# Kernel tuning notes

Hardware: AMD Instinct MI355X
Metric: run time of the kernel (lower is better)

## Reference

```python
import jax, jax.numpy as jnp
import numpy as np


def setup_inputs() -> dict:
    key = jax.random.key(0)
    n, d = 256, 64
    ks = jax.random.split(key, 8)
    x = jax.random.normal(ks[0], (n, d), jnp.float32)
    v = jax.random.normal(ks[1], (n, d), jnp.float32)
    # torch nn.Linear convention: weight shape (out_features, in_features)
    W1 = jax.random.normal(ks[2], (d, d), jnp.float32) * (1.0 / np.sqrt(d))
    b1 = jax.random.normal(ks[3], (d,), jnp.float32) * 0.1
    # W2 scaled small + b2 ~ scaled identity so g = M + M^T is well-conditioned (invertible)
    W2 = jax.random.normal(ks[4], (d * d, d), jnp.float32) * 0.02
    b2 = (3.0 * jnp.eye(d, dtype=jnp.float32)).reshape(d * d) \
         + jax.random.normal(ks[5], (d * d,), jnp.float32) * 0.01
    W3 = jax.random.normal(ks[6], (d, 2 * d), jnp.float32) * (1.0 / np.sqrt(2 * d))
    return {"t": 0, "x": x, "v": v, "W1": W1, "b1": b1, "W2": W2, "b2": b2, "W3": W3}


def reference(t, x, v, W1, b1, W2, b2, W3):
    # Connection_gnew.forward. t is unused (ODE-time placeholder), matching the original.
    n, d = x.shape
    # g network: linear1 -> tanh -> linear2 -> symmetrize
    h = jnp.tanh(x @ W1.T + b1)                      # (n, d)
    M = (h @ W2.T + b2).reshape(n, d, d)             # (n, d, d)
    g = M + jnp.transpose(M, (0, 2, 1))              # symmetric metric (n, d, d)
    g_inv = jnp.linalg.inv(g)
    # Analytic batch jacobian of g_flat wrt x (replaces autograd.functional.jacobian):
    # d M_flat[a]/d x[l] = sum_m W2[a,m] * (1 - h[m]^2) * W1[m,l]; then symmetrize (i<->j).
    s = 1.0 - h * h                                   # tanh' (n, d)
    J = jnp.einsum('am,nm,ml->nal', W2, s, W1).reshape(n, d, d, d)
    J = J + jnp.transpose(J, (0, 2, 1, 3))            # J[n,i,j,l] = d g_{ij} / d x_l
    # einsum('nkl,nijl,njil,nlij->nkij', g_inv, J, J, -J):
    # elementwise triple product over matching indices, then contract l with g_inv.
    T = J * jnp.transpose(J, (0, 2, 1, 3)) * (-jnp.transpose(J, (0, 2, 3, 1)))  # T[n,i,j,l]
    connection = 0.5 * jnp.einsum('nkl,nijl->nkij', g_inv, T)
    # dv[n,k] = -sum_{ij} v_i v_j connection[n,k,i,j]
    dv = -jnp.einsum('ni,nj,nkij->nk', v, v, connection)
    out = jnp.concatenate([v, dv], axis=-1) @ W3.T    # linear3, no bias
    return out
```

## Files before the change

kernel.cpp:

```cpp
#include <hip/hip_runtime.h>
#include <math.h>
#include <stdint.h>


typedef short short8 __attribute__((ext_vector_type(8)));
typedef float f32x4 __attribute__((ext_vector_type(4)));
typedef float f32x2 __attribute__((ext_vector_type(2)));

__device__ __forceinline__ unsigned short f2bf(float f) {
  unsigned int u = __builtin_bit_cast(unsigned int, f);
  u += 0x7fffu + ((u >> 16) & 1u);
  return (unsigned short)(u >> 16);
}

__device__ __forceinline__ short8 as_short8(uint4 u) {
  union { uint4 a; short8 b; } cv; cv.a = u; return cv.b;
}

__device__ __forceinline__ void stage_slab(const unsigned short* gslab,
                                           unsigned short* lbase, int lane) {
  const int srcoff = ((lane >> 3) << 6) + (((lane & 7) ^ (lane >> 3)) << 3);
  const unsigned short* gsrc = gslab + srcoff;
  #pragma unroll
  for (int k = 0; k < 8; ++k) {
    __builtin_amdgcn_global_load_lds(
        (const __attribute__((address_space(1))) unsigned int*)(gsrc + (k << 9)),
        (__attribute__((address_space(3))) unsigned int*)(lbase + (k << 9)),
        16, 0, 0);
  }
}

__global__ __launch_bounds__(256) void prep_kernel(
    const float* __restrict__ W2, const float* __restrict__ W1,
    const float* __restrict__ b2, unsigned short* __restrict__ W2sB,
    float* __restrict__ W1T, float* __restrict__ b2s) {
  const int b = blockIdx.x;
  if (b < 128) {
    int g = b * 256 + threadIdx.x;
    int i = g >> 9, j = (g >> 3) & 63, m8 = (g & 7) << 3;
    const float* pa = &W2[((((i << 6) + j) << 6) + m8)];
    const float* pb = &W2[((((j << 6) + i) << 6) + m8)];
    float4 a0 = *(const float4*)pa, a1 = *(const float4*)(pa + 4);
    float4 b0 = *(const float4*)pb, b1 = *(const float4*)(pb + 4);
    short8 r;
    r[0] = (short)f2bf(a0.x + b0.x); r[1] = (short)f2bf(a0.y + b0.y);
    r[2] = (short)f2bf(a0.z + b0.z); r[3] = (short)f2bf(a0.w + b0.w);
    r[4] = (short)f2bf(a1.x + b1.x); r[5] = (short)f2bf(a1.y + b1.y);
    r[6] = (short)f2bf(a1.z + b1.z); r[7] = (short)f2bf(a1.w + b1.w);
    *(short8*)&W2sB[(size_t)g << 3] = r;
  } else if (b == 128) {
    for (int e = threadIdx.x; e < 4096; e += 256) {
      int l = e >> 6, m = e & 63;
      W1T[e] = W1[(m << 6) + l];
    }
  } else {
    for (int e = threadIdx.x; e < 4096; e += 256) {
      int r = e >> 6, c = e & 63;
      b2s[e] = b2[(r << 6) + c] + b2[(c << 6) + r];
    }
  }
}

__global__ __launch_bounds__(512) void conn_kernel(
    const float* __restrict__ x, const float* __restrict__ v,
    const float* __restrict__ W1, const float* __restrict__ b1,
    const float* __restrict__ W3, const unsigned short* __restrict__ W2sB,
    const float* __restrict__ W1T, const float* __restrict__ b2s,
    float* __restrict__ out) {
  __shared__ __align__(16) unsigned short sAF[8][2][4096];
  __shared__ __align__(16) unsigned short sKT[80 * 80];
  __shared__ __align__(16) float sg[64 * 68];
  __shared__ __align__(16) float sh[64], sv[64], sx[64];

  float* const spq = (float*)sKT;
  float* const sq  = (float*)sKT + 512;
  float* const szz = (float*)sKT + 576;

  const int n = blockIdx.x, t = threadIdx.x;
  const int wv = t >> 6, lane = t & 63, ln15 = lane & 15, quad = lane >> 4;
  const int o8 = t >> 3, s8 = t & 7;

  if (t < 64) sx[t] = x[(n << 6) + t];
  else if (t < 128) sv[t - 64] = v[(n << 6) + (t - 64)];
  for (int e = t; e < 1280; e += 512) sKT[5120 + e] = 0;
  __syncthreads();

  {
    const float* w1r = &W1[(o8 << 6) + (s8 << 3)];
    float4 wa = *(const float4*)w1r, wb = *(const float4*)(w1r + 4);
    float4 xa = *(const float4*)&sx[s8 << 3], xb = *(const float4*)&sx[(s8 << 3) + 4];
    float acc = wa.x * xa.x + wa.y * xa.y + wa.z * xa.z + wa.w * xa.w
              + wb.x * xb.x + wb.y * xb.y + wb.z * xb.z + wb.w * xb.w;
    acc += __shfl_xor(acc, 1);
    acc += __shfl_xor(acc, 2);
    acc += __shfl_xor(acc, 4);
    if (s8 == 0) sh[o8] = tanhf(acc + b1[o8]);
  }
  __syncthreads();

  for (int e = t; e < 4096; e += 512) {
    int m = e & 63, l = e >> 6;
    float hm = sh[m];
    sKT[l * 80 + m] = f2bf((1.f - hm * hm) * W1T[e]);
  }
  if (t < 64) sKT[64 * 80 + t] = f2bf(sh[t]);
  __syncthreads();

  short8 bf[4][2];
  #pragma unroll
  for (int tc = 0; tc < 4; ++tc)
    #pragma unroll
    for (int ks = 0; ks < 2; ++ks)
      bf[tc][ks] = *(const short8*)&sKT[(tc * 16 + ln15) * 80 + ks * 32 + quad * 8];

  f32x2 qacc2[4] = {{0.f, 0.f}, {0.f, 0.f}, {0.f, 0.f}, {0.f, 0.f}};

  const int f0 = (ln15 << 6) + (((quad ^ ln15) & 7) << 3);
  const int extoff = (64 + ln15) * 80 + quad * 8;
  unsigned short* const myAF = &sAF[wv][0][0];
  const unsigned short* const gbase = W2sB + ((size_t)(8 * wv) << 12);

  stage_slab(gbase, myAF, lane);

  #pragma unroll 1
  for (int ii = 0; ii < 8; ++ii) {
    asm volatile("s_waitcnt vmcnt(0)" ::: "memory");
    __builtin_amdgcn_sched_barrier(0);
    if (ii < 7)
      stage_slab(gbase + ((size_t)(ii + 1) << 12), myAF + (((ii & 1) ^ 1) << 12), lane);

    const unsigned short* buf = myAF + ((ii & 1) << 12);
    uint4 af[4][2];
    #pragma unroll
    for (int tc = 0; tc < 4; ++tc) {
      af[tc][0] = *(const uint4*)&buf[(tc << 10) + f0];
      af[tc][1] = *(const uint4*)&buf[(tc << 10) + (f0 ^ 32)];
    }
    const int i = 8 * wv + ii;
    const float vi = sv[i];

    #pragma unroll
    for (int tr = 0; tr < 4; ++tr) {
      short8 a0 = as_short8(af[tr][0]), a1 = as_short8(af[tr][1]);
      f32x4 c1[4], c2[4];
      #pragma unroll
      for (int tc = 0; tc < 4; ++tc) {
        f32x4 z4 = {0.f, 0.f, 0.f, 0.f};
        f32x4 u = __builtin_amdgcn_mfma_f32_16x16x32_bf16(a0, bf[tc][0], z4, 0, 0, 0);
        c1[tc]  = __builtin_amdgcn_mfma_f32_16x16x32_bf16(a1, bf[tc][1], u, 0, 0, 0);
        f32x4 w = __builtin_amdgcn_mfma_f32_16x16x32_bf16(bf[tr][0], as_short8(af[tc][0]), z4, 0, 0, 0);
        c2[tc]  = __builtin_amdgcn_mfma_f32_16x16x32_bf16(bf[tr][1], as_short8(af[tc][1]), w, 0, 0, 0);
      }
      {
        short8 e0 = *(const short8*)&sKT[extoff];
        short8 e1 = *(const short8*)&sKT[extoff + 32];
        f32x4 z4 = {0.f, 0.f, 0.f, 0.f};
        f32x4 u  = __builtin_amdgcn_mfma_f32_16x16x32_bf16(a0, e0, z4, 0, 0, 0);
        f32x4 ce = __builtin_amdgcn_mfma_f32_16x16x32_bf16(a1, e1, u, 0, 0, 0);
        if (ln15 == 0)
          *(f32x4*)&sg[i * 68 + tr * 16 + quad * 4] = ce;
      }
      f32x4 svj = *(const f32x4*)&sv[tr * 16 + quad * 4];
      f32x2 vi2 = {vi, vi};
      f32x2 w01 = f32x2{svj[0], svj[1]} * vi2;
      f32x2 w23 = f32x2{svj[2], svj[3]} * vi2;
      #pragma unroll
      for (int tc = 0; tc < 4; ++tc) {
        f32x2 c101 = {c1[tc][0], c1[tc][1]}, c123 = {c1[tc][2], c1[tc][3]};
        f32x2 c201 = {c2[tc][0], c2[tc][1]}, c223 = {c2[tc][2], c2[tc][3]};
        f32x2 t01 = (c101 * c101) * c201;
        f32x2 t23 = (c123 * c123) * c223;
        qacc2[tc] = __builtin_elementwise_fma(t01, w01, qacc2[tc]);
        qacc2[tc] = __builtin_elementwise_fma(t23, w23, qacc2[tc]);
      }
    }
  }

  #pragma unroll
  for (int tc = 0; tc < 4; ++tc) {
    float s = qacc2[tc][0] + qacc2[tc][1];
    s += __shfl_xor(s, 16, 64);
    s += __shfl_xor(s, 32, 64);
    if (quad == 0) spq[(wv << 6) + tc * 16 + ln15] = s;
  }
  __syncthreads();

  for (int e = t; e < 4096; e += 512)
    sg[(e >> 6) * 68 + (e & 63)] += b2s[e];
  __syncthreads();

  if (t < 64) {
    float s = spq[t] + spq[64 + t] + spq[128 + t] + spq[192 + t]
            + spq[256 + t] + spq[320 + t] + spq[384 + t] + spq[448 + t];
    sq[t] = s;
    szz[t] = s / sg[t * 68 + t];
  }
  __syncthreads();

  if (t < 64) {
    const float* grow = &sg[t * 68];
    f32x4 gr[16];
    #pragma unroll
    for (int cc = 0; cc < 16; ++cc) gr[cc] = *(const f32x4*)&grow[cc << 2];
    const float dinv = 1.f / grow[t];
    const float qr = sq[t];
    float zr = szz[t];
    #pragma unroll 1
    for (int it = 0; it < 14; ++it) {
      float p[8];
      #pragma unroll
      for (int cc = 0; cc < 8; ++cc) {
        f32x4 za_ = *(const f32x4*)&szz[cc << 3];
        f32x4 zb_ = *(const f32x4*)&szz[(cc << 3) + 4];
        f32x4 ga = gr[cc << 1], gb = gr[(cc << 1) + 1];
        float s = ga[0] * za_[0];
        s = fmaf(ga[1], za_[1], s);
        s = fmaf(ga[2], za_[2], s);
        s = fmaf(ga[3], za_[3], s);
        s = fmaf(gb[0], zb_[0], s);
        s = fmaf(gb[1], zb_[1], s);
        s = fmaf(gb[2], zb_[2], s);
        s = fmaf(gb[3], zb_[3], s);
        p[cc] = s;
      }
      float r4 = ((p[0] + p[1]) + (p[2] + p[3])) + ((p[4] + p[5]) + (p[6] + p[7]));
      zr = zr + (qr - r4) * dinv;
      szz[t] = zr;
      __builtin_amdgcn_sched_barrier(0);
    }
  }
  __syncthreads();

  {
    const float* w3r = &W3[o8 << 7];
    float4 wva = *(const float4*)&w3r[s8 << 3];
    float4 wvb = *(const float4*)&w3r[(s8 << 3) + 4];
    float4 wda = *(const float4*)&w3r[64 + (s8 << 3)];
    float4 wdb = *(const float4*)&w3r[64 + (s8 << 3) + 4];
    float4 va = *(const float4*)&sv[s8 << 3], vb = *(const float4*)&sv[(s8 << 3) + 4];
    float4 za = *(const float4*)&szz[s8 << 3], zb = *(const float4*)&szz[(s8 << 3) + 4];
    float acc = wva.x * va.x + wva.y * va.y + wva.z * va.z + wva.w * va.w
              + wvb.x * vb.x + wvb.y * vb.y + wvb.z * vb.z + wvb.w * vb.w
              + 0.5f * (wda.x * za.x + wda.y * za.y + wda.z * za.z + wda.w * za.w
                      + wdb.x * zb.x + wdb.y * zb.y + wdb.z * zb.z + wdb.w * zb.w);
    acc += __shfl_xor(acc, 1);
    acc += __shfl_xor(acc, 2);
    acc += __shfl_xor(acc, 4);
    if (s8 == 0) out[(n << 6) + o8] = acc;
  }
}

extern "C" void kernel_launch(void* const* d_in, const int* in_sizes, int n_in,
                              void* d_out, int out_size, void* d_ws, size_t ws_size,
                              hipStream_t stream) {
  (void)in_sizes; (void)n_in; (void)out_size; (void)ws_size;
  const float* x  = (const float*)d_in[1];
  const float* v  = (const float*)d_in[2];
  const float* W1 = (const float*)d_in[3];
  const float* b1 = (const float*)d_in[4];
  const float* W2 = (const float*)d_in[5];
  const float* b2 = (const float*)d_in[6];
  const float* W3 = (const float*)d_in[7];
  unsigned short* W2sB = (unsigned short*)d_ws;
  float* W1T = (float*)((char*)d_ws + (512 << 10));
  float* b2s = W1T + 4096;

  hipLaunchKernelGGL(prep_kernel, dim3(130), dim3(256), 0, stream,
                     W2, W1, b2, W2sB, W1T, b2s);
  hipLaunchKernelGGL(conn_kernel, dim3(256), dim3(512), 0, stream,
                     x, v, W1, b1, W3, W2sB, W1T, b2s, (float*)d_out);
}
```

Before: 93.22 us.

## Load W2 fragments directly from global, fast tanh, fewer solver iterations

Removes the per-wave LDS double-buffered staging of the symmetrized W2 slabs and reads the MFMA A fragments straight from global memory, freeing a large shared allocation. It replaces tanhf with a clamped exp2-based formula, hoists the v-part of the final W3 product before a barrier, and cuts the Jacobi iterations for the metric solve from 14 to 10. Fewer iterations lower solve accuracy, and global loads lose the explicit prefetch overlap.

```diff
diff --git a/kernel.cpp b/kernel.cpp
--- a/kernel.cpp
+++ b/kernel.cpp
@@ -15,19 +15,6 @@
 
 __device__ __forceinline__ short8 as_short8(uint4 u) {
   union { uint4 a; short8 b; } cv; cv.a = u; return cv.b;
-}
-
-__device__ __forceinline__ void stage_slab(const unsigned short* gslab,
-                                           unsigned short* lbase, int lane) {
-  const int srcoff = ((lane >> 3) << 6) + (((lane & 7) ^ (lane >> 3)) << 3);
-  const unsigned short* gsrc = gslab + srcoff;
-  #pragma unroll
-  for (int k = 0; k < 8; ++k) {
-    __builtin_amdgcn_global_load_lds(
-        (const __attribute__((address_space(1))) unsigned int*)(gsrc + (k << 9)),
-        (__attribute__((address_space(3))) unsigned int*)(lbase + (k << 9)),
-        16, 0, 0);
-  }
 }
 
 __global__ __launch_bounds__(256) void prep_kernel(
@@ -67,7 +54,6 @@
     const float* __restrict__ W3, const unsigned short* __restrict__ W2sB,
     const float* __restrict__ W1T, const float* __restrict__ b2s,
     float* __restrict__ out) {
-  __shared__ __align__(16) unsigned short sAF[8][2][4096];
   __shared__ __align__(16) unsigned short sKT[80 * 80];
   __shared__ __align__(16) float sg[64 * 68];
   __shared__ __align__(16) float sh[64], sv[64], sx[64];
@@ -94,7 +80,12 @@
     acc += __shfl_xor(acc, 1);
     acc += __shfl_xor(acc, 2);
     acc += __shfl_xor(acc, 4);
-    if (s8 == 0) sh[o8] = tanhf(acc + b1[o8]);
+    if (s8 == 0) {
+      float a = acc + b1[o8];
+      a = fminf(10.f, fmaxf(-10.f, a));
+      float e2 = exp2f(a * 2.8853900817779268f);
+      sh[o8] = (e2 - 1.f) / (e2 + 1.f);
+    }
   }
   __syncthreads();
 
@@ -115,26 +106,18 @@
 
   f32x2 qacc2[4] = {{0.f, 0.f}, {0.f, 0.f}, {0.f, 0.f}, {0.f, 0.f}};
 
-  const int f0 = (ln15 << 6) + (((quad ^ ln15) & 7) << 3);
+  const int foff = (ln15 << 6) + quad * 8;
   const int extoff = (64 + ln15) * 80 + quad * 8;
-  unsigned short* const myAF = &sAF[wv][0][0];
   const unsigned short* const gbase = W2sB + ((size_t)(8 * wv) << 12);
-
-  stage_slab(gbase, myAF, lane);
 
   #pragma unroll 1
   for (int ii = 0; ii < 8; ++ii) {
-    asm volatile("s_waitcnt vmcnt(0)" ::: "memory");
-    __builtin_amdgcn_sched_barrier(0);
-    if (ii < 7)
-      stage_slab(gbase + ((size_t)(ii + 1) << 12), myAF + (((ii & 1) ^ 1) << 12), lane);
-
-    const unsigned short* buf = myAF + ((ii & 1) << 12);
+    const unsigned short* sp = gbase + ((size_t)ii << 12);
     uint4 af[4][2];
     #pragma unroll
     for (int tc = 0; tc < 4; ++tc) {
-      af[tc][0] = *(const uint4*)&buf[(tc << 10) + f0];
-      af[tc][1] = *(const uint4*)&buf[(tc << 10) + (f0 ^ 32)];
+      af[tc][0] = *(const uint4*)(sp + (tc << 10) + foff);
+      af[tc][1] = *(const uint4*)(sp + (tc << 10) + foff + 32);
     }
     const int i = 8 * wv + ii;
     const float vi = sv[i];
@@ -183,6 +166,16 @@
     s += __shfl_xor(s, 32, 64);
     if (quad == 0) spq[(wv << 6) + tc * 16 + ln15] = s;
   }
+
+  float accv;
+  {
+    const float* w3r = &W3[o8 << 7];
+    float4 wva = *(const float4*)&w3r[s8 << 3];
+    float4 wvb = *(const float4*)&w3r[(s8 << 3) + 4];
+    float4 va = *(const float4*)&sv[s8 << 3], vb = *(const float4*)&sv[(s8 << 3) + 4];
+    accv = wva.x * va.x + wva.y * va.y + wva.z * va.z + wva.w * va.w
+         + wvb.x * vb.x + wvb.y * vb.y + wvb.z * vb.z + wvb.w * vb.w;
+  }
   __syncthreads();
 
   for (int e = t; e < 4096; e += 512)
@@ -206,7 +199,7 @@
     const float qr = sq[t];
     float zr = szz[t];
     #pragma unroll 1
-    for (int it = 0; it < 14; ++it) {
+    for (int it = 0; it < 10; ++it) {
       float p[8];
       #pragma unroll
       for (int cc = 0; cc < 8; ++cc) {
@@ -233,14 +226,10 @@
 
   {
     const float* w3r = &W3[o8 << 7];
-    float4 wva = *(const float4*)&w3r[s8 << 3];
-    float4 wvb = *(const float4*)&w3r[(s8 << 3) + 4];
     float4 wda = *(const float4*)&w3r[64 + (s8 << 3)];
     float4 wdb = *(const float4*)&w3r[64 + (s8 << 3) + 4];
-    float4 va = *(const float4*)&sv[s8 << 3], vb = *(const float4*)&sv[(s8 << 3) + 4];
     float4 za = *(const float4*)&szz[s8 << 3], zb = *(const float4*)&szz[(s8 << 3) + 4];
-    float acc = wva.x * va.x + wva.y * va.y + wva.z * va.z + wva.w * va.w
-              + wvb.x * vb.x + wvb.y * vb.y + wvb.z * vb.z + wvb.w * vb.w
+    float acc = accv
               + 0.5f * (wda.x * za.x + wda.y * za.y + wda.z * za.z + wda.w * za.w
                       + wdb.x * zb.x + wdb.y * zb.y + wdb.z * zb.z + wdb.w * zb.w);
     acc += __shfl_xor(acc, 1);
```

Measured after the change: 93.09 us. No clear change (-0.1%).
